# Optimization experiments

Measured on AMD Instinct MI355X. Metric: run time of the kernel, lower is better.

Reference implementation:

```python
import jax, jax.numpy as jnp
import numpy as np

N_NODES = 100000   # multiple of 20 (tile factor)
N_BASE = N_NODES // 20
N_EDGES = 3200000  # avg degree 32


def setup_inputs() -> dict:
    key = jax.random.key(0)
    ks = jax.random.split(key, 12)
    x1 = jax.random.normal(ks[0], (N_NODES, 15), dtype=jnp.float32)
    x2 = jax.random.normal(ks[1], (N_BASE, 4), dtype=jnp.float32)
    edges = jax.random.randint(ks[2], (2, N_EDGES), 0, N_NODES, dtype=jnp.int64)
    # params (PyTorch Linear convention: y = x @ W.T + b)
    W1 = jax.random.normal(ks[3], (15, 15), dtype=jnp.float32) * 0.1
    b1 = jax.random.normal(ks[4], (15,), dtype=jnp.float32) * 0.1
    Wg = jax.random.normal(ks[5], (15, 34), dtype=jnp.float32) * 0.1  # GCNConv weight
    bg = jax.random.normal(ks[6], (15,), dtype=jnp.float32) * 0.1
    W3 = jax.random.normal(ks[7], (1, 34), dtype=jnp.float32) * 0.1
    b3 = jax.random.normal(ks[8], (1,), dtype=jnp.float32) * 0.1
    W4 = jax.random.normal(ks[9], (19, 19), dtype=jnp.float32) * 0.1
    b4 = jax.random.normal(ks[10], (19,), dtype=jnp.float32) * 0.1
    return {"x1": x1, "x2": x2, "edges": edges, "W1": W1, "b1": b1,
            "Wg": Wg, "bg": bg, "W3": W3, "b3": b3, "W4": W4, "b4": b4}


def reference(x1, x2, edges, W1, b1, Wg, bg, W3, b3, W4, b4):
    N = x1.shape[0]
    # b = layer4(cat([x1, tile(x2, (20,1))]))
    x2t = jnp.tile(x2, (20, 1))                       # [N, 4]
    b = jnp.concatenate([x1, x2t], axis=1) @ W4.T + b4  # [N, 19]
    a = jax.nn.relu(x1 @ W1.T + b1)                     # [N, 15]

    # GCN normalization with self-loops (PyG GCNConv defaults)
    row = jnp.concatenate([edges[0], jnp.arange(N, dtype=edges.dtype)])
    col = jnp.concatenate([edges[1], jnp.arange(N, dtype=edges.dtype)])
    deg = jax.ops.segment_sum(jnp.ones_like(col, dtype=x1.dtype), col, num_segments=N)
    dinv = jnp.where(deg > 0, deg ** -0.5, 0.0)
    norm = dinv[row] * dinv[col]                       # [E+N]

    for _ in range(5):
        h = jnp.concatenate([a, b], axis=1) @ Wg.T     # [N, 15]
        agg = jax.ops.segment_sum(h[row] * norm[:, None], col, num_segments=N)
        a = jax.nn.relu(agg + bg)

    out = jnp.concatenate([a, b], axis=1) @ W3.T + b3  # [N, 1]
    return jnp.tanh(out.mean())
```

## Files before the change

### kernel.cpp

```cpp
#include <hip/hip_runtime.h>
#include <hip/hip_fp16.h>
#include <math.h>

#define N_NODES 100000
#define N_BASE  5000
#define N_EDGES 3200000
#define NBKT    391
#define CAPB    9472
#define EPB     4096
#define GEB     782

__device__ inline unsigned pkh(float a, float b) {
    return (unsigned)__half_as_ushort(__float2half_rn(a)) |
           ((unsigned)__half_as_ushort(__float2half_rn(b)) << 16);
}

__global__ __launch_bounds__(512) void k_initg(int* __restrict__ gcur, float* __restrict__ bins) {
    int t = threadIdx.x;
    if (t < NBKT) gcur[t] = t * CAPB;
    if (t < 64) bins[t] = 0.0f;
}

__global__ __launch_bounds__(512) void k_bucket(const int* __restrict__ row, const int* __restrict__ col,
                                                int* __restrict__ gcur, unsigned* __restrict__ csr) {
    __shared__ int hist[NBKT], gbase[NBKT], curi[NBKT], excl[NBKT];
    __shared__ int sc[512];
    __shared__ unsigned sdst[EPB];
    __shared__ int sadr[EPB];
    int t = threadIdx.x;
    int e0 = blockIdx.x * EPB;
    int cnt = (N_EDGES - e0 < EPB) ? (N_EDGES - e0) : EPB;
    for (int k = t; k < NBKT; k += 512) hist[k] = 0;
    __syncthreads();
    for (int j = t; j < cnt; j += 512) atomicAdd(&hist[col[e0 + j] >> 8], 1);
    __syncthreads();
    sc[t] = (t < NBKT) ? hist[t] : 0;
    __syncthreads();
    for (int off = 1; off < 512; off <<= 1) {
        int v = (t >= off) ? sc[t - off] : 0;
        __syncthreads();
        sc[t] += v;
        __syncthreads();
    }
    if (t < NBKT) {
        int e = sc[t] - hist[t];
        excl[t] = e;
        curi[t] = e;
        gbase[t] = (hist[t] > 0) ? atomicAdd(&gcur[t], hist[t]) : 0;
    }
    __syncthreads();
    for (int j = t; j < cnt; j += 512) {
        int d = col[e0 + j];
        int s = row[e0 + j];
        int b = d >> 8;
        int pos = atomicAdd(&curi[b], 1);
        sdst[pos] = ((unsigned)(d & 255) << 17) | (unsigned)s;
        sadr[pos] = gbase[b] + (pos - excl[b]);
    }
    __syncthreads();
    for (int j = t; j < cnt; j += 512) csr[sadr[j]] = sdst[j];
}

__global__ __launch_bounds__(1024) void k_sort(const int* __restrict__ gcur, unsigned* __restrict__ csr,
                                               int* __restrict__ rs, int* __restrict__ re,
                                               float* __restrict__ dinv) {
    __shared__ unsigned stage[CAPB];
    __shared__ int hist[256], offs[256], cur[256];
    int t = threadIdx.x, b = blockIdx.x;
    int base = b * CAPB;
    int cnt = gcur[b] - base;
    if (t < 256) hist[t] = 0;
    for (int j = t; j < cnt; j += 1024) stage[j] = csr[base + j];
    __syncthreads();
    for (int j = t; j < cnt; j += 1024) atomicAdd(&hist[stage[j] >> 17], 1);
    __syncthreads();
    if (t < 256) offs[t] = hist[t];
    __syncthreads();
    for (int off = 1; off < 256; off <<= 1) {
        int v = 0;
        if (t < 256 && t >= off) v = offs[t - off];
        __syncthreads();
        if (t < 256) offs[t] += v;
        __syncthreads();
    }
    if (t < 256) {
        int excl = offs[t] - hist[t];
        cur[t] = excl;
        int node = b * 256 + t;
        if (node < N_NODES) {
            rs[node] = base + excl;
            re[node] = base + excl + hist[t];
            dinv[node] = rsqrtf((float)(hist[t] + 1));
        }
    }
    __syncthreads();
    for (int j = t; j < cnt; j += 1024) {
        unsigned p = stage[j];
        int slot = atomicAdd(&cur[p >> 17], 1);
        csr[base + slot] = p & 0x1FFFFu;
    }
}

__global__ __launch_bounds__(256) void k_ab_h(const float* __restrict__ x1, const float* __restrict__ x2,
                                              const float* __restrict__ W1, const float* __restrict__ b1,
                                              const float* __restrict__ W4, const float* __restrict__ b4,
                                              const float* __restrict__ Wg, const float* __restrict__ W3,
                                              const float* __restrict__ dinv,
                                              float* __restrict__ bb, __half* __restrict__ h0,
                                              float* __restrict__ bins) {
    __shared__ float sW1[225], sb1[15], sW4[361], sb4[19], sWg[510], sW3b[19];
    for (int t = threadIdx.x; t < 225; t += 256) sW1[t] = W1[t];
    for (int t = threadIdx.x; t < 361; t += 256) sW4[t] = W4[t];
    for (int t = threadIdx.x; t < 510; t += 256) sWg[t] = Wg[t];
    if (threadIdx.x < 15) sb1[threadIdx.x] = b1[threadIdx.x];
    if (threadIdx.x < 19) { sb4[threadIdx.x] = b4[threadIdx.x]; sW3b[threadIdx.x] = W3[15 + threadIdx.x]; }
    __syncthreads();
    int i = blockIdx.x * 256 + threadIdx.x;
    bool valid = i < N_NODES;
    int ii = valid ? i : 0;
    float x[15];
#pragma unroll
    for (int k = 0; k < 15; k++) x[k] = x1[(size_t)ii * 15 + k];
    float xt[4];
    int ib = ii % N_BASE;
#pragma unroll
    for (int k = 0; k < 4; k++) xt[k] = x2[(size_t)ib * 4 + k];
    float in[34];
    float bp = 0.0f;
#pragma unroll
    for (int o = 0; o < 19; o++) {
        float s = sb4[o];
#pragma unroll
        for (int k = 0; k < 15; k++) s += x[k] * sW4[o * 19 + k];
#pragma unroll
        for (int k = 0; k < 4; k++) s += xt[k] * sW4[o * 19 + 15 + k];
        in[15 + o] = s;
        bp += s * sW3b[o];
    }
#pragma unroll
    for (int o = 0; o < 15; o++) {
        float s = sb1[o];
#pragma unroll
        for (int k = 0; k < 15; k++) s += x[k] * sW1[o * 15 + k];
        in[o] = fmaxf(s, 0.0f);
    }
    float dn = dinv[ii];
    if (valid) {
        float4* bbp = (float4*)(bb + (size_t)ii * 20);
        bbp[0] = make_float4(in[15], in[16], in[17], in[18]);
        bbp[1] = make_float4(in[19], in[20], in[21], in[22]);
        bbp[2] = make_float4(in[23], in[24], in[25], in[26]);
        bbp[3] = make_float4(in[27], in[28], in[29], in[30]);
        bbp[4] = make_float4(in[31], in[32], in[33], 0.0f);
        float hv[15];
#pragma unroll
        for (int o = 0; o < 15; o++) {
            float s = 0.0f;
#pragma unroll
            for (int k = 0; k < 34; k++) s += in[k] * sWg[o * 34 + k];
            hv[o] = s * dn;
        }
        unsigned hu[8];
#pragma unroll
        for (int k = 0; k < 7; k++) hu[k] = pkh(hv[2 * k], hv[2 * k + 1]);
        hu[7] = pkh(hv[14], 0.0f);
        uint4* hp = (uint4*)(h0 + (size_t)ii * 16);
        hp[0] = make_uint4(hu[0], hu[1], hu[2], hu[3]);
        hp[1] = make_uint4(hu[4], hu[5], hu[6], hu[7]);
    }
    float val = valid ? bp : 0.0f;
#pragma unroll
    for (int off = 32; off > 0; off >>= 1) val += __shfl_down(val, off, 64);
    __shared__ float wsum[4];
    if ((threadIdx.x & 63) == 0) wsum[threadIdx.x >> 6] = val;
    __syncthreads();
    if (threadIdx.x == 0) atomicAdd(&bins[blockIdx.x & 63], wsum[0] + wsum[1] + wsum[2] + wsum[3]);
}

__global__ __launch_bounds__(1024) void k_gather(const int* __restrict__ rs, const int* __restrict__ re,
                                                 const unsigned* __restrict__ csr,
                                                 const __half* __restrict__ h_in,
                                                 const float* __restrict__ dinv,
                                                 const float* __restrict__ bb,
                                                 const float* __restrict__ Wg,
                                                 const float* __restrict__ bg,
                                                 const float* __restrict__ W3,
                                                 __half* __restrict__ h_out,
                                                 float* __restrict__ bins, int last) {
    __shared__ float sWg[544], sbg[16], sW3[16];
    __shared__ float ws2[16];
    int t = threadIdx.x;
    for (int k = t; k < 544; k += 1024) sWg[k] = (k < 510) ? Wg[k] : 0.0f;
    if (t < 16) { sbg[t] = (t < 15) ? bg[t] : 0.0f; sW3[t] = (t < 15) ? W3[t] : 0.0f; }
    __syncthreads();
    int node = blockIdx.x * 16 + (t >> 6);
    int lane = t & 63, c2 = lane & 7, p = lane >> 3;
    int start = rs[node];
    int deg = re[node] - start;
    const unsigned* hp = (const unsigned*)h_in;
    unsigned hsu = hp[(size_t)node * 8 + c2];
    float accx = 0.0f, accy = 0.0f;
    for (int base = 0; base < deg; base += 64) {
        int rem = deg - base;
        unsigned ce = 0;
        if (lane < rem) ce = csr[start + base + lane];
        int lim = rem < 64 ? rem : 64;
        unsigned tmp[8];
#pragma unroll
        for (int i = 0; i < 8; i++) {
            int e0 = p + 8 * i;
            unsigned pk = __shfl(ce, e0, 64);
            tmp[i] = (e0 < lim) ? hp[(size_t)(pk & 0x1FFFFu) * 8 + c2] : 0u;
        }
#pragma unroll
        for (int i = 0; i < 8; i++) {
            float2 f = __half22float2(*(__half2*)&tmp[i]);
            accx += f.x;
            accy += f.y;
        }
    }
    accx += __shfl_xor(accx, 8, 64);
    accy += __shfl_xor(accy, 8, 64);
    accx += __shfl_xor(accx, 16, 64);
    accy += __shfl_xor(accy, 16, 64);
    accx += __shfl_xor(accx, 32, 64);
    accy += __shfl_xor(accy, 32, 64);
    float dn = dinv[node];
    float2 hsf = __half22float2(*(__half2*)&hsu);
    float avx = fmaxf(dn * (hsf.x + accx) + sbg[2 * c2], 0.0f);
    float avy = fmaxf(dn * (hsf.y + accy) + sbg[2 * c2 + 1], 0.0f);
    if (!last) {
        int o0 = 2 * c2;
        float ix0 = __shfl(avx, p >> 1, 64);
        float iy0 = __shfl(avy, p >> 1, 64);
        float ix1 = __shfl(avx, (p + 8) >> 1, 64);
        float iy1 = __shfl(avy, (p + 8) >> 1, 64);
        float inv0 = (p & 1) ? iy0 : ix0;
        float inv1 = (p & 1) ? iy1 : ix1;
        if (p == 7) inv1 = bb[(size_t)node * 20 + 0];
        float s0 = inv0 * sWg[o0 * 34 + p]       + inv1 * sWg[o0 * 34 + p + 8];
        float s1 = inv0 * sWg[(o0 + 1) * 34 + p] + inv1 * sWg[(o0 + 1) * 34 + p + 8];
#pragma unroll
        for (int i = 2; i < 5; i++) {
            int k = p + 8 * i;
            if (k < 34) {
                float inv = bb[(size_t)node * 20 + (k - 15)];
                s0 += inv * sWg[o0 * 34 + k];
                s1 += inv * sWg[(o0 + 1) * 34 + k];
            }
        }
        s0 += __shfl_xor(s0, 8, 64);
        s1 += __shfl_xor(s1, 8, 64);
        s0 += __shfl_xor(s0, 16, 64);
        s1 += __shfl_xor(s1, 16, 64);
        s0 += __shfl_xor(s0, 32, 64);
        s1 += __shfl_xor(s1, 32, 64);
        if (p == 0)
            ((unsigned*)h_out)[(size_t)node * 8 + c2] = pkh(s0 * dn, s1 * dn);
    } else {
        float c = avx * sW3[2 * c2] + avy * sW3[2 * c2 + 1];
        c += __shfl_xor(c, 1, 64);
        c += __shfl_xor(c, 2, 64);
        c += __shfl_xor(c, 4, 64);
        if ((t & 63) == 0) ws2[t >> 6] = c;
        __syncthreads();
        if (t == 0) {
            float s = 0.0f;
#pragma unroll
            for (int k = 0; k < 16; k++) s += ws2[k];
            atomicAdd(&bins[blockIdx.x & 63], s);
        }
    }
}

__global__ void k_finalize(const float* __restrict__ bins, const float* __restrict__ b3,
                           float* __restrict__ out) {
    float s = 0.0f;
    for (int k = 0; k < 64; k++) s += bins[k];
    out[0] = tanhf(s * (1.0f / (float)N_NODES) + b3[0]);
}

extern "C" void kernel_launch(void* const* d_in, const int* in_sizes, int n_in,
                              void* d_out, int out_size, void* d_ws, size_t ws_size,
                              hipStream_t stream) {
    const float* x1 = (const float*)d_in[0];
    const float* x2 = (const float*)d_in[1];
    const int* edges = (const int*)d_in[2];
    const float* W1 = (const float*)d_in[3];
    const float* b1 = (const float*)d_in[4];
    const float* Wg = (const float*)d_in[5];
    const float* bg = (const float*)d_in[6];
    const float* W3 = (const float*)d_in[7];
    const float* b3 = (const float*)d_in[8];
    const float* W4 = (const float*)d_in[9];
    const float* b4 = (const float*)d_in[10];

    const int* row = edges;
    const int* col = edges + N_EDGES;

    char* ws = (char*)d_ws;
    unsigned* csr  = (unsigned*)ws;
    float*    bb   = (float*)(csr + (size_t)NBKT * CAPB);
    __half*   h0   = (__half*)(bb + (size_t)N_NODES * 20);
    __half*   h1   = h0 + (size_t)N_NODES * 16;
    float*    dinv = (float*)(h1 + (size_t)N_NODES * 16);
    int*      rs   = (int*)(dinv + N_NODES);
    int*      re   = rs + N_NODES;
    int*      gcur = re + N_NODES;
    float*    bins = (float*)(gcur + NBKT);

    int gN = (N_NODES + 255) / 256;

    k_initg<<<1, 512, 0, stream>>>(gcur, bins);
    k_bucket<<<GEB, 512, 0, stream>>>(row, col, gcur, csr);
    k_sort<<<NBKT, 1024, 0, stream>>>(gcur, csr, rs, re, dinv);
    k_ab_h<<<gN, 256, 0, stream>>>(x1, x2, W1, b1, W4, b4, Wg, W3, dinv, bb, h0, bins);
    for (int t = 0; t < 5; t++) {
        const __half* hi = (t & 1) ? h1 : h0;
        __half* ho = (t & 1) ? h0 : h1;
        k_gather<<<N_NODES / 16, 1024, 0, stream>>>(rs, re, csr, hi, dinv, bb, Wg, bg, W3,
                                                    ho, bins, t == 4 ? 1 : 0);
    }
    k_finalize<<<1, 1, 0, stream>>>(bins, b3, (float*)d_out);
}
```

Before: 389.2 us.

## Gather neighbor rows with 16-byte loads and accumulate in packed half2

The neighbor gather now has each pair of lanes fetch one whole 32-byte fp16 node row as two uint4 loads, so 32 edges are in flight per wave-iteration instead of 8 lanes each loading 4 bytes. Accumulation moves from fp32 to packed half2 adds, and a butterfly shuffle reduction leaves the 8 channel pairs spread across lanes. The aggregated features are then passed through shared memory for the dense Wg projection. This cuts load instruction count and shuffle overhead in the memory-bound gather, but fp16 accumulation over about 33 terms loses precision and adds a block-wide sync.

```diff
diff --git a/kernel.cpp b/kernel.cpp
--- a/kernel.cpp
+++ b/kernel.cpp
@@ -13,6 +13,11 @@
 __device__ inline unsigned pkh(float a, float b) {
     return (unsigned)__half_as_ushort(__float2half_rn(a)) |
            ((unsigned)__half_as_ushort(__float2half_rn(b)) << 16);
+}
+
+__device__ inline unsigned hadd2u(unsigned a, unsigned b) {
+    __half2 r = __hadd2(*(__half2*)&a, *(__half2*)&b);
+    return *(unsigned*)&r;
 }
 
 __global__ __launch_bounds__(512) void k_initg(int* __restrict__ gcur, float* __restrict__ bins) {
@@ -188,81 +193,94 @@
                                                  __half* __restrict__ h_out,
                                                  float* __restrict__ bins, int last) {
     __shared__ float sWg[544], sbg[16], sW3[16];
+    __shared__ float sa[16][16];
     __shared__ float ws2[16];
     int t = threadIdx.x;
     for (int k = t; k < 544; k += 1024) sWg[k] = (k < 510) ? Wg[k] : 0.0f;
     if (t < 16) { sbg[t] = (t < 15) ? bg[t] : 0.0f; sW3[t] = (t < 15) ? W3[t] : 0.0f; }
     __syncthreads();
-    int node = blockIdx.x * 16 + (t >> 6);
-    int lane = t & 63, c2 = lane & 7, p = lane >> 3;
+    int wid = t >> 6;
+    int node = blockIdx.x * 16 + wid;
+    int lane = t & 63, es = lane >> 1, half = lane & 1;
     int start = rs[node];
     int deg = re[node] - start;
-    const unsigned* hp = (const unsigned*)h_in;
-    unsigned hsu = hp[(size_t)node * 8 + c2];
-    float accx = 0.0f, accy = 0.0f;
+    const uint4* hp4 = (const uint4*)h_in;
+    uint4 sv = make_uint4(0u, 0u, 0u, 0u);
+    if (es == 0) sv = hp4[(size_t)node * 2 + half];
+    unsigned a0 = sv.x, a1 = sv.y, a2 = sv.z, a3 = sv.w;
     for (int base = 0; base < deg; base += 64) {
         int rem = deg - base;
+        int lim = rem < 64 ? rem : 64;
         unsigned ce = 0;
-        if (lane < rem) ce = csr[start + base + lane];
-        int lim = rem < 64 ? rem : 64;
-        unsigned tmp[8];
-#pragma unroll
-        for (int i = 0; i < 8; i++) {
-            int e0 = p + 8 * i;
-            unsigned pk = __shfl(ce, e0, 64);
-            tmp[i] = (e0 < lim) ? hp[(size_t)(pk & 0x1FFFFu) * 8 + c2] : 0u;
-        }
-#pragma unroll
-        for (int i = 0; i < 8; i++) {
-            float2 f = __half22float2(*(__half2*)&tmp[i]);
-            accx += f.x;
-            accy += f.y;
-        }
-    }
-    accx += __shfl_xor(accx, 8, 64);
-    accy += __shfl_xor(accy, 8, 64);
-    accx += __shfl_xor(accx, 16, 64);
-    accy += __shfl_xor(accy, 16, 64);
-    accx += __shfl_xor(accx, 32, 64);
-    accy += __shfl_xor(accy, 32, 64);
+        if (lane < lim) ce = csr[start + base + lane];
+        unsigned pa = __shfl(ce, es, 64);
+        uint4 va = make_uint4(0u, 0u, 0u, 0u);
+        if (es < lim) va = hp4[(size_t)pa * 2 + half];
+        if (lim > 32) {
+            unsigned pb = __shfl(ce, es + 32, 64);
+            uint4 vb = make_uint4(0u, 0u, 0u, 0u);
+            if (es + 32 < lim) vb = hp4[(size_t)pb * 2 + half];
+            a0 = hadd2u(a0, va.x); a1 = hadd2u(a1, va.y);
+            a2 = hadd2u(a2, va.z); a3 = hadd2u(a3, va.w);
+            a0 = hadd2u(a0, vb.x); a1 = hadd2u(a1, vb.y);
+            a2 = hadd2u(a2, vb.z); a3 = hadd2u(a3, vb.w);
+        } else {
+            a0 = hadd2u(a0, va.x); a1 = hadd2u(a1, va.y);
+            a2 = hadd2u(a2, va.z); a3 = hadd2u(a3, va.w);
+        }
+    }
+    int sel2 = (lane >> 1) & 1;
+    unsigned s0 = sel2 ? a0 : a2;
+    unsigned s1 = sel2 ? a1 : a3;
+    unsigned k0 = sel2 ? a2 : a0;
+    unsigned k1 = sel2 ? a3 : a1;
+    k0 = hadd2u(k0, __shfl_xor(s0, 2, 64));
+    k1 = hadd2u(k1, __shfl_xor(s1, 2, 64));
+    int sel4 = (lane >> 2) & 1;
+    unsigned sd = sel4 ? k0 : k1;
+    unsigned kk = sel4 ? k1 : k0;
+    kk = hadd2u(kk, __shfl_xor(sd, 4, 64));
+    kk = hadd2u(kk, __shfl_xor(kk, 8, 64));
+    kk = hadd2u(kk, __shfl_xor(kk, 16, 64));
+    kk = hadd2u(kk, __shfl_xor(kk, 32, 64));
+    int pr = 4 * half + 2 * sel2 + sel4;
+    float2 fsum = __half22float2(*(__half2*)&kk);
     float dn = dinv[node];
-    float2 hsf = __half22float2(*(__half2*)&hsu);
-    float avx = fmaxf(dn * (hsf.x + accx) + sbg[2 * c2], 0.0f);
-    float avy = fmaxf(dn * (hsf.y + accy) + sbg[2 * c2 + 1], 0.0f);
+    float avx = fmaxf(dn * fsum.x + sbg[2 * pr], 0.0f);
+    float avy = fmaxf(dn * fsum.y + sbg[2 * pr + 1], 0.0f);
+    if (lane < 8) { sa[wid][2 * pr] = avx; sa[wid][2 * pr + 1] = avy; }
+    __syncthreads();
     if (!last) {
-        int o0 = 2 * c2;
-        float ix0 = __shfl(avx, p >> 1, 64);
-        float iy0 = __shfl(avy, p >> 1, 64);
-        float ix1 = __shfl(avx, (p + 8) >> 1, 64);
-        float iy1 = __shfl(avy, (p + 8) >> 1, 64);
-        float inv0 = (p & 1) ? iy0 : ix0;
-        float inv1 = (p & 1) ? iy1 : ix1;
-        if (p == 7) inv1 = bb[(size_t)node * 20 + 0];
-        float s0 = inv0 * sWg[o0 * 34 + p]       + inv1 * sWg[o0 * 34 + p + 8];
-        float s1 = inv0 * sWg[(o0 + 1) * 34 + p] + inv1 * sWg[(o0 + 1) * 34 + p + 8];
+        int c2e = lane & 7, p = lane >> 3;
+        int o0 = 2 * c2e;
+        float inv0 = sa[wid][p];
+        float inv1 = (p < 7) ? sa[wid][p + 8] : bb[(size_t)node * 20 + 0];
+        float s0e = inv0 * sWg[o0 * 34 + p]       + inv1 * sWg[o0 * 34 + p + 8];
+        float s1e = inv0 * sWg[(o0 + 1) * 34 + p] + inv1 * sWg[(o0 + 1) * 34 + p + 8];
 #pragma unroll
         for (int i = 2; i < 5; i++) {
             int k = p + 8 * i;
             if (k < 34) {
                 float inv = bb[(size_t)node * 20 + (k - 15)];
-                s0 += inv * sWg[o0 * 34 + k];
-                s1 += inv * sWg[(o0 + 1) * 34 + k];
+                s0e += inv * sWg[o0 * 34 + k];
+                s1e += inv * sWg[(o0 + 1) * 34 + k];
             }
         }
-        s0 += __shfl_xor(s0, 8, 64);
-        s1 += __shfl_xor(s1, 8, 64);
-        s0 += __shfl_xor(s0, 16, 64);
-        s1 += __shfl_xor(s1, 16, 64);
-        s0 += __shfl_xor(s0, 32, 64);
-        s1 += __shfl_xor(s1, 32, 64);
+        s0e += __shfl_xor(s0e, 8, 64);
+        s1e += __shfl_xor(s1e, 8, 64);
+        s0e += __shfl_xor(s0e, 16, 64);
+        s1e += __shfl_xor(s1e, 16, 64);
+        s0e += __shfl_xor(s0e, 32, 64);
+        s1e += __shfl_xor(s1e, 32, 64);
         if (p == 0)
-            ((unsigned*)h_out)[(size_t)node * 8 + c2] = pkh(s0 * dn, s1 * dn);
+            ((unsigned*)h_out)[(size_t)node * 8 + c2e] = pkh(s0e * dn, s1e * dn);
     } else {
-        float c = avx * sW3[2 * c2] + avy * sW3[2 * c2 + 1];
+        float c = 0.0f;
+        if (lane < 8) c = avx * sW3[2 * pr] + avy * sW3[2 * pr + 1];
         c += __shfl_xor(c, 1, 64);
         c += __shfl_xor(c, 2, 64);
         c += __shfl_xor(c, 4, 64);
-        if ((t & 63) == 0) ws2[t >> 6] = c;
+        if (lane == 0) ws2[wid] = c;
         __syncthreads();
         if (t == 0) {
             float s = 0.0f;
```

Result: slower. 400.4 us (+2.9%).
